# Performance work log

Hardware: AMD Instinct MI355X
Metric: run time of the kernel (lower is better)

The kernel has to match this reference:

```python
import jax, jax.numpy as jnp
import numpy as np

D_MODEL = 768
D_STATE = 64
EXPAND = 2
HEADDIM = 64
D_INNER = EXPAND * D_MODEL            # 1536
NHEADS = D_INNER // HEADDIM           # 24
CONV_CH = D_INNER + 2 * D_STATE       # 1664 (ngroups=1)
D_IN_PROJ = 2 * D_INNER + 2 * D_STATE + NHEADS  # 3224
SEQ_LEN = 256
BATCH = 8
D_CONV = 4
EPS = 1e-5


def setup_inputs() -> dict:
    key = jax.random.key(0)
    ks = jax.random.split(key, 8)
    seq = jax.random.normal(ks[0], (SEQ_LEN, BATCH, D_MODEL), dtype=jnp.float32)
    W_in = jax.random.normal(ks[1], (D_MODEL, D_IN_PROJ), dtype=jnp.float32) * (D_MODEL ** -0.5)
    conv_w = jax.random.uniform(ks[2], (CONV_CH, D_CONV), dtype=jnp.float32, minval=-0.5, maxval=0.5)
    conv_b = jax.random.uniform(ks[3], (CONV_CH,), dtype=jnp.float32, minval=-0.1, maxval=0.1)
    # dt bias so softplus(dt) lands in a reasonable range
    dt_bias = jax.random.uniform(ks[4], (NHEADS,), dtype=jnp.float32, minval=-4.0, maxval=-1.0)
    # A = -exp(A_log), A_log ~ log(U[1,16]) per Mamba2 init
    A_log = jnp.log(jax.random.uniform(ks[5], (NHEADS,), dtype=jnp.float32, minval=1.0, maxval=16.0))
    D = jnp.ones((NHEADS,), dtype=jnp.float32) + 0.1 * jax.random.normal(ks[6], (NHEADS,), dtype=jnp.float32)
    norm_w = jnp.ones((D_INNER,), dtype=jnp.float32)
    W_out = jax.random.normal(ks[7], (D_INNER, D_MODEL), dtype=jnp.float32) * (D_INNER ** -0.5)
    return {"seq": seq, "W_in": W_in, "conv_w": conv_w, "conv_b": conv_b,
            "dt_bias": dt_bias, "A_log": A_log, "D": D, "norm_w": norm_w, "W_out": W_out}


def _mamba_scan(seq, W_in, conv_w, conv_b, dt_bias, A_log, D, norm_w, W_out):
    B = seq.shape[1]
    A = -jnp.exp(A_log)                      # [H]
    w_last = conv_w[:, -1]                   # per-step conv sees only current token

    def step(h, x_t):                        # h: [B,H,P,N], x_t: [B,D_MODEL]
        zxbcdt = x_t @ W_in                  # [B, D_IN_PROJ]
        z = zxbcdt[:, :D_INNER]
        xBC = zxbcdt[:, D_INNER:D_INNER + CONV_CH]
        dt = zxbcdt[:, D_INNER + CONV_CH:]   # [B, H]
        xBC = jax.nn.silu(xBC * w_last + conv_b)
        x = xBC[:, :D_INNER].reshape(B, NHEADS, HEADDIM)   # [B,H,P]
        Bm = xBC[:, D_INNER:D_INNER + D_STATE]             # [B,N]
        Cm = xBC[:, D_INNER + D_STATE:]                    # [B,N]
        dt = jax.nn.softplus(dt + dt_bias)                 # [B,H]
        dA = jnp.exp(dt * A)                               # [B,H]
        # h' = dA * h + dt * x (outer) B
        h = h * dA[:, :, None, None] + (dt[:, :, None] * x)[..., None] * Bm[:, None, None, :]
        y = jnp.einsum('bhpn,bn->bhp', h, Cm) + D[None, :, None] * x
        y = y.reshape(B, D_INNER) * jax.nn.silu(z)         # gate
        y = y * jax.lax.rsqrt(jnp.mean(y * y, axis=-1, keepdims=True) + EPS) * norm_w
        out = y @ W_out                                    # [B, D_MODEL]
        return h, (out, h)

    h0 = jnp.zeros((B, NHEADS, HEADDIM, D_STATE), dtype=seq.dtype)
    _, (outputs, states) = jax.lax.scan(step, h0, seq)
    return outputs, states


def reference(seq, W_in, conv_w, conv_b, dt_bias, A_log, D, norm_w, W_out):
    # outputs: [S, B, d_model]; states: [S, B, H, P, N] (final SSM state per step)
    return _mamba_scan(seq, W_in, conv_w, conv_b, dt_bias, A_log, D, norm_w, W_out)
```

## Files before the change

kernel.cpp:

```cpp
#include <hip/hip_runtime.h>
#include <cstdint>
#include <cstddef>

#define SEQ_LEN 256
#define BATCH 8
#define D_MODEL 768
#define D_STATE 64
#define HEADDIM 64
#define D_INNER 1536
#define NHEADS 24
#define CONV_CH 1664
#define D_IN_PROJ 3224
#define ZXLD 3328
#define ROWS (SEQ_LEN*BATCH)

typedef float   f32x4 __attribute__((ext_vector_type(4)));
typedef _Float16 f16x8 __attribute__((ext_vector_type(8)));
typedef _Float16 f16x4 __attribute__((ext_vector_type(4)));

__device__ __forceinline__ float silu_f(float v) { return v / (1.f + __expf(-v)); }

__device__ __forceinline__ void gl_lds16(const _Float16* g, _Float16* l) {
  __builtin_amdgcn_global_load_lds(
      (const __attribute__((address_space(1))) unsigned int*)g,
      (__attribute__((address_space(3))) unsigned int*)l, 16, 0, 0);
}

__global__ __launch_bounds__(256) void cast_f16_kernel(
    const float* __restrict__ in, _Float16* __restrict__ out, int n4)
{
  int i = blockIdx.x * 256 + threadIdx.x;
  if (i >= n4) return;
  f32x4 v = ((const f32x4*)in)[i];
  f16x4 o;
  o[0] = (_Float16)v[0]; o[1] = (_Float16)v[1];
  o[2] = (_Float16)v[2]; o[3] = (_Float16)v[3];
  ((f16x4*)out)[i] = o;
}

__global__ __launch_bounds__(256) void transpose_cast_kernel(
    const float* __restrict__ in, _Float16* __restrict__ out, int R, int C, int Cpad)
{
  __shared__ float tile[32][33];
  int c0 = blockIdx.x * 32, r0 = blockIdx.y * 32;
  int tc = threadIdx.x & 31, tr = threadIdx.x >> 5;
#pragma unroll
  for (int i = 0; i < 4; i++) {
    int r = r0 + tr + i * 8, c = c0 + tc;
    tile[tr + i * 8][tc] = (r < R && c < C) ? in[(size_t)r * C + c] : 0.f;
  }
  __syncthreads();
#pragma unroll
  for (int i = 0; i < 4; i++) {
    int oc  = c0 + tr + i * 8;
    int orr = r0 + tc;
    if (oc < Cpad && orr < R) out[(size_t)oc * R + orr] = (_Float16)tile[tc][tr + i * 8];
  }
}

#define BKG 64
__global__ __launch_bounds__(256) void gemm_f16_glds(
    const _Float16* __restrict__ A, const _Float16* __restrict__ Bt,
    float* __restrict__ C, int M, int N, int K)
{
  __shared__ __align__(16) _Float16 As[128 * BKG];
  __shared__ __align__(16) _Float16 Bs[128 * BKG];
  int tid = threadIdx.x;
  int m0 = blockIdx.x * 128, n0 = blockIdx.y * 128;
  int wave = tid >> 6, lane = tid & 63;
  int wm = (wave >> 1) * 64, wn = (wave & 1) * 64;
  int lr = lane & 15, lk = lane >> 4;

  int srow[4], scol[4];
#pragma unroll
  for (int i = 0; i < 4; i++) {
    int o = wave * 4096 + i * 1024 + lane * 16;
    int row = o >> 7, cp = (o >> 4) & 7;
    srow[i] = row;
    scol[i] = (cp ^ (row & 7)) * 8;
  }

  f32x4 z4 = {0.f, 0.f, 0.f, 0.f};
  f32x4 acc[4][4];
#pragma unroll
  for (int i = 0; i < 4; i++)
#pragma unroll
    for (int j = 0; j < 4; j++) acc[i][j] = z4;

  for (int k0 = 0; k0 < K; k0 += BKG) {
#pragma unroll
    for (int i = 0; i < 4; i++) {
      gl_lds16(A  + (size_t)(m0 + srow[i]) * K + k0 + scol[i],
               As + wave * 2048 + i * 512);
      gl_lds16(Bt + (size_t)(n0 + srow[i]) * K + k0 + scol[i],
               Bs + wave * 2048 + i * 512);
    }
    __syncthreads();
#pragma unroll
    for (int kk = 0; kk < 2; kk++) {
      f16x8 af[4], bfv[4];
#pragma unroll
      for (int i = 0; i < 4; i++) {
        int row = wm + i * 16 + lr;
        int ch  = (kk * 4 + lk) ^ (row & 7);
        af[i] = *(const f16x8*)(As + row * BKG + ch * 8);
      }
#pragma unroll
      for (int j = 0; j < 4; j++) {
        int row = wn + j * 16 + lr;
        int ch  = (kk * 4 + lk) ^ (row & 7);
        bfv[j] = *(const f16x8*)(Bs + row * BKG + ch * 8);
      }
#pragma unroll
      for (int i = 0; i < 4; i++)
#pragma unroll
        for (int j = 0; j < 4; j++)
          acc[i][j] = __builtin_amdgcn_mfma_f32_16x16x32_f16(af[i], bfv[j], acc[i][j], 0, 0, 0);
    }
    __syncthreads();
  }
#pragma unroll
  for (int i = 0; i < 4; i++)
#pragma unroll
    for (int j = 0; j < 4; j++) {
      int col = n0 + wn + j * 16 + lr;
#pragma unroll
      for (int r = 0; r < 4; r++) {
        int row = m0 + wm + i * 16 + lk * 4 + r;
        C[(size_t)row * N + col] = acc[i][j][r];
      }
    }
}

__global__ __launch_bounds__(256) void prep_kernel(
    const float* __restrict__ zx,
    const float* __restrict__ conv_w,
    const float* __restrict__ conv_b,
    const float* __restrict__ dt_bias,
    const float* __restrict__ A_log,
    const float* __restrict__ Dp,
    float* __restrict__ siluBC,
    float* __restrict__ coefX,
    float* __restrict__ dxX,
    float* __restrict__ dAr)
{
  int r = blockIdx.x;
  int tid = threadIdx.x;
  const float* row = zx + (size_t)r * ZXLD;
  __shared__ float sdtp[NHEADS];
  if (tid < NHEADS) {
    float dtr = row[D_INNER + CONV_CH + tid] + dt_bias[tid];
    float dtp = (dtr > 15.f) ? dtr : log1pf(__expf(dtr));
    sdtp[tid] = dtp;
    float Ar = -__expf(A_log[tid]);
    dAr[(size_t)r * NHEADS + tid] = __expf(dtp * Ar);
  }
  if (tid < 128) {
    int ch = D_INNER + tid;
    float v = row[2 * D_INNER + tid] * conv_w[ch * 4 + 3] + conv_b[ch];
    siluBC[(size_t)r * 128 + tid] = silu_f(v);
  }
  __syncthreads();
#pragma unroll
  for (int i = 0; i < 6; i++) {
    int c = tid + i * 256;
    float xv = silu_f(row[D_INNER + c] * conv_w[c * 4 + 3] + conv_b[c]);
    int h = c >> 6;
    coefX[(size_t)r * D_INNER + c] = sdtp[h] * xv;
    dxX[(size_t)r * D_INNER + c]  = Dp[h] * xv;
  }
}

__global__ __launch_bounds__(256) void scan2_kernel(
    const float* __restrict__ siluBC,
    const float* __restrict__ coefX,
    const float* __restrict__ dAr,
    const float* __restrict__ dxX,
    float* __restrict__ states,
    float* __restrict__ y_raw)
{
  int g = blockIdx.x;
  int bh = g >> 2, qp = g & 3;
  int b = bh / NHEADS, hh = bh - b * NHEADS;
  int tid = threadIdx.x;
  int pp = tid >> 4, nq = tid & 15;
  int n0 = nq * 4;
  int p  = qp * 16 + pp;
  int chp = hh * HEADDIM + p;

  f32x4 h4 = {0.f, 0.f, 0.f, 0.f};

  f32x4 aB, aC, bB, bC;
  float aCo, adA, aDx, bCo, bdA, bDx;
  {
    int r = b;
    aB  = *(const f32x4*)(siluBC + (size_t)r * 128 + n0);
    aC  = *(const f32x4*)(siluBC + (size_t)r * 128 + 64 + n0);
    aCo = coefX[(size_t)r * D_INNER + chp];
    adA = dAr[(size_t)r * NHEADS + hh];
    aDx = dxX[(size_t)r * D_INNER + chp];
    r = BATCH + b;
    bB  = *(const f32x4*)(siluBC + (size_t)r * 128 + n0);
    bC  = *(const f32x4*)(siluBC + (size_t)r * 128 + 64 + n0);
    bCo = coefX[(size_t)r * D_INNER + chp];
    bdA = dAr[(size_t)r * NHEADS + hh];
    bDx = dxX[(size_t)r * D_INNER + chp];
  }

  for (int t = 0; t < SEQ_LEN; t += 2) {
    {
      int r = t * BATCH + b;
#pragma unroll
      for (int q = 0; q < 4; q++) h4[q] = h4[q] * adA + aCo * aB[q];
      float* sp = states + ((size_t)r * NHEADS + hh) * 4096 + (size_t)p * 64 + n0;
      __builtin_nontemporal_store(h4, (f32x4*)sp);
      float acc = h4[0] * aC[0] + h4[1] * aC[1] + h4[2] * aC[2] + h4[3] * aC[3];
      acc += __shfl_xor(acc, 1);
      acc += __shfl_xor(acc, 2);
      acc += __shfl_xor(acc, 4);
      acc += __shfl_xor(acc, 8);
      if (nq == 0) y_raw[(size_t)r * D_INNER + chp] = acc + aDx;
      if (t + 2 < SEQ_LEN) {
        int rn = (t + 2) * BATCH + b;
        aB  = *(const f32x4*)(siluBC + (size_t)rn * 128 + n0);
        aC  = *(const f32x4*)(siluBC + (size_t)rn * 128 + 64 + n0);
        aCo = coefX[(size_t)rn * D_INNER + chp];
        adA = dAr[(size_t)rn * NHEADS + hh];
        aDx = dxX[(size_t)rn * D_INNER + chp];
      }
    }
    {
      int r = (t + 1) * BATCH + b;
#pragma unroll
      for (int q = 0; q < 4; q++) h4[q] = h4[q] * bdA + bCo * bB[q];
      float* sp = states + ((size_t)r * NHEADS + hh) * 4096 + (size_t)p * 64 + n0;
      __builtin_nontemporal_store(h4, (f32x4*)sp);
      float acc = h4[0] * bC[0] + h4[1] * bC[1] + h4[2] * bC[2] + h4[3] * bC[3];
      acc += __shfl_xor(acc, 1);
      acc += __shfl_xor(acc, 2);
      acc += __shfl_xor(acc, 4);
      acc += __shfl_xor(acc, 8);
      if (nq == 0) y_raw[(size_t)r * D_INNER + chp] = acc + bDx;
      if (t + 3 < SEQ_LEN) {
        int rn = (t + 3) * BATCH + b;
        bB  = *(const f32x4*)(siluBC + (size_t)rn * 128 + n0);
        bC  = *(const f32x4*)(siluBC + (size_t)rn * 128 + 64 + n0);
        bCo = coefX[(size_t)rn * D_INNER + chp];
        bdA = dAr[(size_t)rn * NHEADS + hh];
        bDx = dxX[(size_t)rn * D_INNER + chp];
      }
    }
  }
}

__global__ __launch_bounds__(256) void gate_norm_kernel(
    const float* __restrict__ zx, const float* __restrict__ y_raw,
    const float* __restrict__ norm_w, _Float16* __restrict__ yh)
{
  int r = blockIdx.x;
  const float* z = zx + (size_t)r * ZXLD;
  const float* y = y_raw + (size_t)r * D_INNER;
  float v[6];
  float ss = 0.f;
#pragma unroll
  for (int i = 0; i < 6; i++) {
    int c = threadIdx.x + i * 256;
    float w = y[c] * silu_f(z[c]);
    v[i] = w;
    ss += w * w;
  }
#pragma unroll
  for (int o = 32; o > 0; o >>= 1) ss += __shfl_xor(ss, o);
  __shared__ float red[4];
  if ((threadIdx.x & 63) == 0) red[threadIdx.x >> 6] = ss;
  __syncthreads();
  float tot = red[0] + red[1] + red[2] + red[3];
  float scale = rsqrtf(tot / (float)D_INNER + 1e-5f);
#pragma unroll
  for (int i = 0; i < 6; i++) {
    int c = threadIdx.x + i * 256;
    yh[(size_t)r * D_INNER + c] = (_Float16)(v[i] * scale * norm_w[c]);
  }
}

extern "C" void kernel_launch(void* const* d_in, const int* in_sizes, int n_in,
                              void* d_out, int out_size, void* d_ws, size_t ws_size,
                              hipStream_t stream)
{
  (void)in_sizes; (void)n_in; (void)out_size; (void)ws_size;
  const float* seq     = (const float*)d_in[0];
  const float* W_in    = (const float*)d_in[1];
  const float* conv_w  = (const float*)d_in[2];
  const float* conv_b  = (const float*)d_in[3];
  const float* dt_bias = (const float*)d_in[4];
  const float* A_log   = (const float*)d_in[5];
  const float* Dp      = (const float*)d_in[6];
  const float* norm_w  = (const float*)d_in[7];
  const float* W_out   = (const float*)d_in[8];

  float* out    = (float*)d_out;
  float* states = out + (size_t)SEQ_LEN * BATCH * D_MODEL;

  char* ws = (char*)d_ws;
  size_t off = 0;
  auto alloc = [&](size_t bytes) -> void* {
    void* p = ws + off;
    off = (off + bytes + 255) & ~(size_t)255;
    return p;
  };
  float*    zx     = (float*)   alloc((size_t)ROWS * ZXLD * 4);
  float*    y_raw  = (float*)   alloc((size_t)ROWS * D_INNER * 4);
  _Float16* seqh   = (_Float16*)alloc((size_t)ROWS * D_MODEL * 2);
  _Float16* WinT   = (_Float16*)alloc((size_t)ZXLD * D_MODEL * 2);
  _Float16* WoutT  = (_Float16*)alloc((size_t)D_MODEL * D_INNER * 2);
  _Float16* yh     = (_Float16*)alloc((size_t)ROWS * D_INNER * 2);
  float*    siluBC = (float*)   alloc((size_t)ROWS * 128 * 4);
  float*    coefX  = (float*)   alloc((size_t)ROWS * D_INNER * 4);
  float*    dxX    = (float*)   alloc((size_t)ROWS * D_INNER * 4);
  float*    dAr    = (float*)   alloc((size_t)ROWS * NHEADS * 4);

  cast_f16_kernel<<<(ROWS * D_MODEL / 4 + 255) / 256, 256, 0, stream>>>(
      seq, seqh, ROWS * D_MODEL / 4);
  transpose_cast_kernel<<<dim3(ZXLD / 32, (D_MODEL + 31) / 32), 256, 0, stream>>>(
      W_in, WinT, D_MODEL, D_IN_PROJ, ZXLD);
  transpose_cast_kernel<<<dim3(D_MODEL / 32, (D_INNER + 31) / 32), 256, 0, stream>>>(
      W_out, WoutT, D_INNER, D_MODEL, D_MODEL);

  gemm_f16_glds<<<dim3(ROWS / 128, ZXLD / 128), 256, 0, stream>>>(
      seqh, WinT, zx, ROWS, ZXLD, D_MODEL);

  prep_kernel<<<ROWS, 256, 0, stream>>>(
      zx, conv_w, conv_b, dt_bias, A_log, Dp, siluBC, coefX, dxX, dAr);

  scan2_kernel<<<BATCH * NHEADS * 4, 256, 0, stream>>>(
      siluBC, coefX, dAr, dxX, states, y_raw);

  gate_norm_kernel<<<ROWS, 256, 0, stream>>>(zx, y_raw, norm_w, yh);

  gemm_f16_glds<<<dim3(ROWS / 128, D_MODEL / 128), 256, 0, stream>>>(
      yh, WoutT, out, ROWS, D_MODEL, D_INNER);
}
```

Baseline: 217.3 us.

## Fuse prep into scan kernel and merge cast/transpose launches into one

Removes the separate prep kernel by computing the conv, silu, softplus and decay terms inside the scan loop straight from the projection output, so the intermediate siluBC, coefX, dxX and dAr buffers are never written or read back. The cast kernel and the two weight transpose-cast kernels are merged into a single launch that dispatches on block index, cutting launch count. The cost is that the serial scan now does more transcendental math per step (the same silu values are recomputed by many threads), which lengthens the latency-bound recurrence.

```diff
diff --git a/kernel.cpp b/kernel.cpp
--- a/kernel.cpp
+++ b/kernel.cpp
@@ -26,24 +26,40 @@
       (__attribute__((address_space(3))) unsigned int*)l, 16, 0, 0);
 }
 
-__global__ __launch_bounds__(256) void cast_f16_kernel(
-    const float* __restrict__ in, _Float16* __restrict__ out, int n4)
-{
-  int i = blockIdx.x * 256 + threadIdx.x;
-  if (i >= n4) return;
-  f32x4 v = ((const f32x4*)in)[i];
-  f16x4 o;
-  o[0] = (_Float16)v[0]; o[1] = (_Float16)v[1];
-  o[2] = (_Float16)v[2]; o[3] = (_Float16)v[3];
-  ((f16x4*)out)[i] = o;
-}
-
-__global__ __launch_bounds__(256) void transpose_cast_kernel(
-    const float* __restrict__ in, _Float16* __restrict__ out, int R, int C, int Cpad)
+#define CAST_BLKS 1536
+#define TW1_X 104
+#define TW1_BLKS (TW1_X*24)
+#define TW2_X 24
+#define TW2_BLKS (TW2_X*48)
+__global__ __launch_bounds__(256) void pre_fused_kernel(
+    const float* __restrict__ seq, _Float16* __restrict__ seqh,
+    const float* __restrict__ W_in, _Float16* __restrict__ WinT,
+    const float* __restrict__ W_out, _Float16* __restrict__ WoutT)
 {
   __shared__ float tile[32][33];
-  int c0 = blockIdx.x * 32, r0 = blockIdx.y * 32;
-  int tc = threadIdx.x & 31, tr = threadIdx.x >> 5;
+  int bid = blockIdx.x;
+  int tid = threadIdx.x;
+  if (bid < CAST_BLKS) {
+    int i = bid * 256 + tid;
+    f32x4 v = ((const f32x4*)seq)[i];
+    f16x4 o;
+    o[0] = (_Float16)v[0]; o[1] = (_Float16)v[1];
+    o[2] = (_Float16)v[2]; o[3] = (_Float16)v[3];
+    ((f16x4*)seqh)[i] = o;
+    return;
+  }
+  const float* in; _Float16* out; int R, C, Cpad, bx, by;
+  if (bid < CAST_BLKS + TW1_BLKS) {
+    int b2 = bid - CAST_BLKS;
+    bx = b2 % TW1_X; by = b2 / TW1_X;
+    in = W_in; out = WinT; R = D_MODEL; C = D_IN_PROJ; Cpad = ZXLD;
+  } else {
+    int b2 = bid - CAST_BLKS - TW1_BLKS;
+    bx = b2 % TW2_X; by = b2 / TW2_X;
+    in = W_out; out = WoutT; R = D_INNER; C = D_MODEL; Cpad = D_MODEL;
+  }
+  int c0 = bx * 32, r0 = by * 32;
+  int tc = tid & 31, tr = tid >> 5;
 #pragma unroll
   for (int i = 0; i < 4; i++) {
     int r = r0 + tr + i * 8, c = c0 + tc;
@@ -132,50 +148,13 @@
     }
 }
 
-__global__ __launch_bounds__(256) void prep_kernel(
+__global__ __launch_bounds__(256) void scan3_kernel(
     const float* __restrict__ zx,
     const float* __restrict__ conv_w,
     const float* __restrict__ conv_b,
     const float* __restrict__ dt_bias,
     const float* __restrict__ A_log,
     const float* __restrict__ Dp,
-    float* __restrict__ siluBC,
-    float* __restrict__ coefX,
-    float* __restrict__ dxX,
-    float* __restrict__ dAr)
-{
-  int r = blockIdx.x;
-  int tid = threadIdx.x;
-  const float* row = zx + (size_t)r * ZXLD;
-  __shared__ float sdtp[NHEADS];
-  if (tid < NHEADS) {
-    float dtr = row[D_INNER + CONV_CH + tid] + dt_bias[tid];
-    float dtp = (dtr > 15.f) ? dtr : log1pf(__expf(dtr));
-    sdtp[tid] = dtp;
-    float Ar = -__expf(A_log[tid]);
-    dAr[(size_t)r * NHEADS + tid] = __expf(dtp * Ar);
-  }
-  if (tid < 128) {
-    int ch = D_INNER + tid;
-    float v = row[2 * D_INNER + tid] * conv_w[ch * 4 + 3] + conv_b[ch];
-    siluBC[(size_t)r * 128 + tid] = silu_f(v);
-  }
-  __syncthreads();
-#pragma unroll
-  for (int i = 0; i < 6; i++) {
-    int c = tid + i * 256;
-    float xv = silu_f(row[D_INNER + c] * conv_w[c * 4 + 3] + conv_b[c]);
-    int h = c >> 6;
-    coefX[(size_t)r * D_INNER + c] = sdtp[h] * xv;
-    dxX[(size_t)r * D_INNER + c]  = Dp[h] * xv;
-  }
-}
-
-__global__ __launch_bounds__(256) void scan2_kernel(
-    const float* __restrict__ siluBC,
-    const float* __restrict__ coefX,
-    const float* __restrict__ dAr,
-    const float* __restrict__ dxX,
     float* __restrict__ states,
     float* __restrict__ y_raw)
 {
@@ -188,66 +167,95 @@
   int p  = qp * 16 + pp;
   int chp = hh * HEADDIM + p;
 
+  float wlx = conv_w[chp * 4 + 3], cbx = conv_b[chp];
+  float wB[4], bB[4], wC[4], bC[4];
+#pragma unroll
+  for (int i = 0; i < 4; i++) {
+    int chB = D_INNER + n0 + i;
+    int chC = D_INNER + 64 + n0 + i;
+    wB[i] = conv_w[chB * 4 + 3]; bB[i] = conv_b[chB];
+    wC[i] = conv_w[chC * 4 + 3]; bC[i] = conv_b[chC];
+  }
+  float dtb = dt_bias[hh];
+  float Ar  = -__expf(A_log[hh]);
+  float Dr  = Dp[hh];
+
   f32x4 h4 = {0.f, 0.f, 0.f, 0.f};
 
-  f32x4 aB, aC, bB, bC;
-  float aCo, adA, aDx, bCo, bdA, bDx;
+  f32x4 aB, aC, bB4, bC4;
+  float ax, adt, bx, bdt;
   {
-    int r = b;
-    aB  = *(const f32x4*)(siluBC + (size_t)r * 128 + n0);
-    aC  = *(const f32x4*)(siluBC + (size_t)r * 128 + 64 + n0);
-    aCo = coefX[(size_t)r * D_INNER + chp];
-    adA = dAr[(size_t)r * NHEADS + hh];
-    aDx = dxX[(size_t)r * D_INNER + chp];
-    r = BATCH + b;
-    bB  = *(const f32x4*)(siluBC + (size_t)r * 128 + n0);
-    bC  = *(const f32x4*)(siluBC + (size_t)r * 128 + 64 + n0);
-    bCo = coefX[(size_t)r * D_INNER + chp];
-    bdA = dAr[(size_t)r * NHEADS + hh];
-    bDx = dxX[(size_t)r * D_INNER + chp];
+    const float* r0p = zx + (size_t)b * ZXLD;
+    aB  = *(const f32x4*)(r0p + 2 * D_INNER + n0);
+    aC  = *(const f32x4*)(r0p + 2 * D_INNER + 64 + n0);
+    ax  = r0p[D_INNER + chp];
+    adt = r0p[2 * D_INNER + 2 * D_STATE + hh];
+    const float* r1p = zx + (size_t)(BATCH + b) * ZXLD;
+    bB4 = *(const f32x4*)(r1p + 2 * D_INNER + n0);
+    bC4 = *(const f32x4*)(r1p + 2 * D_INNER + 64 + n0);
+    bx  = r1p[D_INNER + chp];
+    bdt = r1p[2 * D_INNER + 2 * D_STATE + hh];
   }
 
   for (int t = 0; t < SEQ_LEN; t += 2) {
     {
       int r = t * BATCH + b;
-#pragma unroll
-      for (int q = 0; q < 4; q++) h4[q] = h4[q] * adA + aCo * aB[q];
+      float xv  = silu_f(ax * wlx + cbx);
+      float dtr = adt + dtb;
+      float dtp = (dtr > 15.f) ? dtr : log1pf(__expf(dtr));
+      float dA  = __expf(dtp * Ar);
+      float coef = dtp * xv;
+      float acc = 0.f;
+#pragma unroll
+      for (int q = 0; q < 4; q++) {
+        float Bq = silu_f(aB[q] * wB[q] + bB[q]);
+        h4[q] = h4[q] * dA + coef * Bq;
+        float Cq = silu_f(aC[q] * wC[q] + bC[q]);
+        acc += h4[q] * Cq;
+      }
       float* sp = states + ((size_t)r * NHEADS + hh) * 4096 + (size_t)p * 64 + n0;
       __builtin_nontemporal_store(h4, (f32x4*)sp);
-      float acc = h4[0] * aC[0] + h4[1] * aC[1] + h4[2] * aC[2] + h4[3] * aC[3];
       acc += __shfl_xor(acc, 1);
       acc += __shfl_xor(acc, 2);
       acc += __shfl_xor(acc, 4);
       acc += __shfl_xor(acc, 8);
-      if (nq == 0) y_raw[(size_t)r * D_INNER + chp] = acc + aDx;
+      if (nq == 0) y_raw[(size_t)r * D_INNER + chp] = acc + Dr * xv;
       if (t + 2 < SEQ_LEN) {
-        int rn = (t + 2) * BATCH + b;
-        aB  = *(const f32x4*)(siluBC + (size_t)rn * 128 + n0);
-        aC  = *(const f32x4*)(siluBC + (size_t)rn * 128 + 64 + n0);
-        aCo = coefX[(size_t)rn * D_INNER + chp];
-        adA = dAr[(size_t)rn * NHEADS + hh];
-        aDx = dxX[(size_t)rn * D_INNER + chp];
+        const float* rp = zx + (size_t)((t + 2) * BATCH + b) * ZXLD;
+        aB  = *(const f32x4*)(rp + 2 * D_INNER + n0);
+        aC  = *(const f32x4*)(rp + 2 * D_INNER + 64 + n0);
+        ax  = rp[D_INNER + chp];
+        adt = rp[2 * D_INNER + 2 * D_STATE + hh];
       }
     }
     {
       int r = (t + 1) * BATCH + b;
-#pragma unroll
-      for (int q = 0; q < 4; q++) h4[q] = h4[q] * bdA + bCo * bB[q];
+      float xv  = silu_f(bx * wlx + cbx);
+      float dtr = bdt + dtb;
+      float dtp = (dtr > 15.f) ? dtr : log1pf(__expf(dtr));
+      float dA  = __expf(dtp * Ar);
+      float coef = dtp * xv;
+      float acc = 0.f;
+#pragma unroll
+      for (int q = 0; q < 4; q++) {
+        float Bq = silu_f(bB4[q] * wB[q] + bB[q]);
+        h4[q] = h4[q] * dA + coef * Bq;
+        float Cq = silu_f(bC4[q] * wC[q] + bC[q]);
+        acc += h4[q] * Cq;
+      }
       float* sp = states + ((size_t)r * NHEADS + hh) * 4096 + (size_t)p * 64 + n0;
       __builtin_nontemporal_store(h4, (f32x4*)sp);
-      float acc = h4[0] * bC[0] + h4[1] * bC[1] + h4[2] * bC[2] + h4[3] * bC[3];
       acc += __shfl_xor(acc, 1);
       acc += __shfl_xor(acc, 2);
       acc += __shfl_xor(acc, 4);
       acc += __shfl_xor(acc, 8);
-      if (nq == 0) y_raw[(size_t)r * D_INNER + chp] = acc + bDx;
+      if (nq == 0) y_raw[(size_t)r * D_INNER + chp] = acc + Dr * xv;
       if (t + 3 < SEQ_LEN) {
-        int rn = (t + 3) * BATCH + b;
-        bB  = *(const f32x4*)(siluBC + (size_t)rn * 128 + n0);
-        bC  = *(const f32x4*)(siluBC + (size_t)rn * 128 + 64 + n0);
-        bCo = coefX[(size_t)rn * D_INNER + chp];
-        bdA = dAr[(size_t)rn * NHEADS + hh];
-        bDx = dxX[(size_t)rn * D_INNER + chp];
+        const float* rp = zx + (size_t)((t + 3) * BATCH + b) * ZXLD;
+        bB4 = *(const f32x4*)(rp + 2 * D_INNER + n0);
+        bC4 = *(const f32x4*)(rp + 2 * D_INNER + 64 + n0);
+        bx  = rp[D_INNER + chp];
+        bdt = rp[2 * D_INNER + 2 * D_STATE + hh];
       }
     }
   }
@@ -314,26 +322,15 @@
   _Float16* WinT   = (_Float16*)alloc((size_t)ZXLD * D_MODEL * 2);
   _Float16* WoutT  = (_Float16*)alloc((size_t)D_MODEL * D_INNER * 2);
   _Float16* yh     = (_Float16*)alloc((size_t)ROWS * D_INNER * 2);
-  float*    siluBC = (float*)   alloc((size_t)ROWS * 128 * 4);
-  float*    coefX  = (float*)   alloc((size_t)ROWS * D_INNER * 4);
-  float*    dxX    = (float*)   alloc((size_t)ROWS * D_INNER * 4);
-  float*    dAr    = (float*)   alloc((size_t)ROWS * NHEADS * 4);
-
-  cast_f16_kernel<<<(ROWS * D_MODEL / 4 + 255) / 256, 256, 0, stream>>>(
-      seq, seqh, ROWS * D_MODEL / 4);
-  transpose_cast_kernel<<<dim3(ZXLD / 32, (D_MODEL + 31) / 32), 256, 0, stream>>>(
-      W_in, WinT, D_MODEL, D_IN_PROJ, ZXLD);
-  transpose_cast_kernel<<<dim3(D_MODEL / 32, (D_INNER + 31) / 32), 256, 0, stream>>>(
-      W_out, WoutT, D_INNER, D_MODEL, D_MODEL);
+
+  pre_fused_kernel<<<CAST_BLKS + TW1_BLKS + TW2_BLKS, 256, 0, stream>>>(
+      seq, seqh, W_in, WinT, W_out, WoutT);
 
   gemm_f16_glds<<<dim3(ROWS / 128, ZXLD / 128), 256, 0, stream>>>(
       seqh, WinT, zx, ROWS, ZXLD, D_MODEL);
 
-  prep_kernel<<<ROWS, 256, 0, stream>>>(
-      zx, conv_w, conv_b, dt_bias, A_log, Dp, siluBC, coefX, dxX, dAr);
-
-  scan2_kernel<<<BATCH * NHEADS * 4, 256, 0, stream>>>(
-      siluBC, coefX, dAr, dxX, states, y_raw);
+  scan3_kernel<<<BATCH * NHEADS * 4, 256, 0, stream>>>(
+      zx, conv_w, conv_b, dt_bias, A_log, Dp, states, y_raw);
 
   gate_norm_kernel<<<ROWS, 256, 0, stream>>>(zx, y_raw, norm_w, yh);
 
```

New measurement: 490.3 us. 2.26x slower.
